# Kernel tuning notes

Hardware: AMD Instinct MI355X
Metric: run time of the kernel (lower is better)

Reference implementation:

```python
import jax, jax.numpy as jnp
import numpy as np

N_EMBD = 512
N_HEAD = 8
N_INPUTS = 3
HEAD = N_EMBD // N_HEAD


def setup_inputs() -> dict:
    key = jax.random.key(0)
    ks = jax.random.split(key, 12)
    B, T1, T2, C, NI = 2, 2048, 2048, N_EMBD, N_INPUTS
    s = 0.02
    return {
        "x": jax.random.normal(ks[0], (B, T1, C), jnp.float32),
        "y": jax.random.normal(ks[1], (NI, B, T2, C), jnp.float32),
        "Wq": jax.random.normal(ks[2], (C, C), jnp.float32) * s,
        "bq": jnp.zeros((C,), jnp.float32),
        "Wk": jax.random.normal(ks[3], (NI, C, C), jnp.float32) * s,
        "bk": jnp.zeros((NI, C), jnp.float32),
        "Wv": jax.random.normal(ks[4], (NI, C, C), jnp.float32) * s,
        "bv": jnp.zeros((NI, C), jnp.float32),
        "Wp": jax.random.normal(ks[5], (C, C), jnp.float32) * s,
        "bp": jnp.zeros((C,), jnp.float32),
    }


def reference(x, y, Wq, bq, Wk, bk, Wv, bv, Wp, bp):
    B, T1, C = x.shape
    H, D = N_HEAD, HEAD
    # q: [B,H,T1,D], pre-scaled by 1/sqrt(D) as in the original
    q = (x @ Wq + bq).reshape(B, T1, H, D).transpose(0, 2, 1, 3)
    q = q / jnp.sqrt(jnp.asarray(D, q.dtype))
    out = jnp.zeros_like(q)
    for i in range(N_INPUTS):  # small fixed loop over distinct K/V sources
        yi = y[i]
        T2 = yi.shape[1]
        k = (yi @ Wk[i] + bk[i]).reshape(B, T2, H, D).transpose(0, 2, 1, 3)
        v = (yi @ Wv[i] + bv[i]).reshape(B, T2, H, D).transpose(0, 2, 1, 3)
        attn = jax.nn.softmax(jnp.einsum('bhqd,bhkd->bhqk', q, k), axis=-1)
        out = out + jnp.einsum('bhqk,bhkd->bhqd', attn, v)
    out = out.transpose(0, 2, 1, 3).reshape(B, T1, C)
    return out @ Wp + bp
```

## Files before the change

### kernel.cpp

```cpp
#include <hip/hip_runtime.h>

typedef __attribute__((ext_vector_type(8))) __bf16 bf16x8;
typedef __attribute__((ext_vector_type(4))) __bf16 bf16x4;
typedef __attribute__((ext_vector_type(4))) float f32x4;
typedef __attribute__((ext_vector_type(8))) unsigned short us8;

__device__ __forceinline__ unsigned short f2b(float f) {
    unsigned int u = __builtin_bit_cast(unsigned int, f);
    u = (u + 0x7fffu + ((u >> 16) & 1u)) >> 16;
    return (unsigned short)u;
}
__device__ __forceinline__ float b2f(unsigned short u) {
    return __builtin_bit_cast(float, (unsigned int)u << 16);
}
__device__ __forceinline__ float exp2fast(float x) {
    return __builtin_amdgcn_exp2f(x);
}
__device__ __forceinline__ void gload16(const void* g, void* l) {
    __builtin_amdgcn_global_load_lds(
        (const __attribute__((address_space(1))) unsigned int*)g,
        (__attribute__((address_space(3))) unsigned int*)l, 16, 0, 0);
}

#define LOG2E 1.44269504088896f

__global__ void prep_w(const float* __restrict__ Wq, const float* __restrict__ Wk,
                       const float* __restrict__ Wv, const float* __restrict__ Wp,
                       unsigned short* __restrict__ Wt) {
    __shared__ float tile[64][65];
    int w = blockIdx.z;
    const float* src = (w == 0) ? Wq
                     : (w < 4)  ? Wk + (size_t)(w - 1) * 512 * 512
                     : (w < 7)  ? Wv + (size_t)(w - 4) * 512 * 512
                                : Wp;
    int n0 = blockIdx.x * 64, k0 = blockIdx.y * 64;
    int t = threadIdx.x;
    int rr = t >> 4, c4 = (t & 15) * 4;
#pragma unroll
    for (int j = 0; j < 4; j++) {
        int r = rr + j * 16;
        float4 v = *(const float4*)(src + (size_t)(k0 + r) * 512 + n0 + c4);
        tile[r][c4 + 0] = v.x; tile[r][c4 + 1] = v.y;
        tile[r][c4 + 2] = v.z; tile[r][c4 + 3] = v.w;
    }
    __syncthreads();
#pragma unroll
    for (int j = 0; j < 4; j++) {
        int rn = rr + j * 16;
        ushort4 o;
        o.x = f2b(tile[c4 + 0][rn]); o.y = f2b(tile[c4 + 1][rn]);
        o.z = f2b(tile[c4 + 2][rn]); o.w = f2b(tile[c4 + 3][rn]);
        *(ushort4*)(Wt + (size_t)w * 512 * 512 + (size_t)(n0 + rn) * 512 + k0 + c4) = o;
    }
}

template <int MODE>
__global__ __launch_bounds__(256, 3) void gemm_k(
    const float* __restrict__ x, const float* __restrict__ y,
    const unsigned short* __restrict__ Wt,
    const float* __restrict__ bq, const float* __restrict__ bk, const float* __restrict__ bv,
    unsigned short* __restrict__ Qb, unsigned short* __restrict__ Kb, unsigned short* __restrict__ Vb,
    const unsigned short* __restrict__ aob, const float* __restrict__ bp, float* __restrict__ outf) {
    __shared__ unsigned short As[128 * 64];
    __shared__ unsigned short Bs[128 * 64];

    int bid = blockIdx.x;
    int CHUNK = (MODE == 0) ? 112 : 16;
    int w = (bid & 7) * CHUNK + (bid >> 3);
    int z, mq, nq;
    if (MODE == 0) {
        z = w >> 7;
        int rem = w & 127;
        mq = rem >> 2; nq = rem & 3;
    } else {
        z = 0; mq = w >> 2; nq = w & 3;
    }

    const float* A = nullptr;
    const unsigned short* W;
    const float* bias;
    unsigned short* outb = nullptr;
    float scale = 1.f;
    if (MODE == 0) {
        if (z == 0) {
            A = x; W = Wt; bias = bq; outb = Qb; scale = 0.125f * LOG2E;
        } else if (z < 4) {
            int i = z - 1;
            A = y + (size_t)i * 4096 * 512;
            W = Wt + (size_t)z * 512 * 512;
            bias = bk + i * 512;
            outb = Kb + (size_t)i * 4096 * 512;
        } else {
            int i = z - 4;
            A = y + (size_t)i * 4096 * 512;
            W = Wt + (size_t)z * 512 * 512;
            bias = bv + i * 512;
            outb = Vb + (size_t)i * 4096 * 512;
        }
    } else {
        W = Wt + (size_t)7 * 512 * 512; bias = bp;
    }

    int m0 = mq * 128, n0 = nq * 128;
    int t = threadIdx.x;
    int lane = t & 63, wid = t >> 6;
    int lg = lane >> 4, lr = lane & 15;
    int wm = wid >> 1, wn = wid & 1;
    int ssl = lane & 7, srow8 = lane >> 3;

    f32x4 acc[4][4];
    const f32x4 zf = {0.f, 0.f, 0.f, 0.f};
#pragma unroll
    for (int mi = 0; mi < 4; mi++)
#pragma unroll
        for (int ni = 0; ni < 4; ni++) acc[mi][ni] = zf;

    for (int kt = 0; kt < 8; ++kt) {
        float4 av[8];
        if (MODE == 0) {
#pragma unroll
            for (int j = 0; j < 8; j++) {
                int c = t + 256 * j;
                int row = c >> 4, kq = c & 15;
                av[j] = *(const float4*)(A + (size_t)(m0 + row) * 512 + kt * 64 + kq * 4);
            }
        }
        __syncthreads();
#pragma unroll
        for (int j = 0; j < 4; j++) {
            int row = (j * 4 + wid) * 8 + srow8;
            gload16(W + (size_t)(n0 + row) * 512 + kt * 64 + ((ssl ^ (row & 7)) * 8),
                    Bs + (j * 4 + wid) * 512);
        }
        if (MODE == 0) {
#pragma unroll
            for (int j = 0; j < 8; j++) {
                int c = t + 256 * j;
                int row = c >> 4, kq = c & 15;
                float4 v = av[j];
                bf16x4 o4 = {(__bf16)v.x, (__bf16)v.y, (__bf16)v.z, (__bf16)v.w};
                *(bf16x4*)(As + row * 64 + (((kq >> 1) ^ (row & 7)) * 8) + (kq & 1) * 4) = o4;
            }
        } else {
#pragma unroll
            for (int j = 0; j < 4; j++) {
                int c = t + 256 * j;
                int row = c >> 3, sl = c & 7;
                const unsigned short* p0 = aob + (size_t)(m0 + row) * 512 + kt * 64 + sl * 8;
                us8 a0 = *(const us8*)p0;
                us8 a1 = *(const us8*)(p0 + (size_t)4096 * 512);
                us8 a2 = *(const us8*)(p0 + (size_t)2 * 4096 * 512);
                bf16x8 o8;
#pragma unroll
                for (int e = 0; e < 8; e++)
                    o8[e] = (__bf16)(b2f(a0[e]) + b2f(a1[e]) + b2f(a2[e]));
                *(bf16x8*)(As + row * 64 + ((sl ^ (row & 7)) * 8)) = o8;
            }
        }
        __syncthreads();

        bf16x8 af[4][2];
#pragma unroll
        for (int mi = 0; mi < 4; mi++)
#pragma unroll
            for (int kk = 0; kk < 2; kk++) {
                int row = wm * 64 + mi * 16 + lr;
                int sl = (kk * 4 + lg) ^ (row & 7);
                af[mi][kk] = *(const bf16x8*)(As + row * 64 + sl * 8);
            }
        __builtin_amdgcn_s_setprio(1);
#pragma unroll
        for (int ni = 0; ni < 4; ni++)
#pragma unroll
            for (int kk = 0; kk < 2; kk++) {
                int row = wn * 64 + ni * 16 + lr;
                int sl = (kk * 4 + lg) ^ (row & 7);
                bf16x8 bf = *(const bf16x8*)(Bs + row * 64 + sl * 8);
#pragma unroll
                for (int mi = 0; mi < 4; mi++)
                    acc[mi][ni] = __builtin_amdgcn_mfma_f32_16x16x32_bf16(af[mi][kk], bf, acc[mi][ni], 0, 0, 0);
            }
        __builtin_amdgcn_s_setprio(0);
    }

#pragma unroll
    for (int ni = 0; ni < 4; ni++) {
        int col = n0 + wn * 64 + ni * 16 + lr;
        float bb = bias[col];
#pragma unroll
        for (int mi = 0; mi < 4; mi++) {
            int row0 = m0 + wm * 64 + mi * 16 + lg * 4;
#pragma unroll
            for (int r = 0; r < 4; r++) {
                float v = (acc[mi][ni][r] + bb) * scale;
                if (MODE == 0)
                    outb[(size_t)(row0 + r) * 512 + col] = __builtin_bit_cast(unsigned short, (__bf16)v);
                else
                    outf[(size_t)(row0 + r) * 512 + col] = v;
            }
        }
    }
}

__global__ void transpose_v(const unsigned short* __restrict__ Vb,
                            unsigned short* __restrict__ Vt) {
    __shared__ unsigned short tile[64][68];
    int i = blockIdx.z, bh = blockIdx.y, t20 = blockIdx.x * 64;
    int b = bh >> 3, h = bh & 7;
    int t = threadIdx.x;
    int rr = t >> 4, c4 = (t & 15) * 4;
    const unsigned short* src = Vb + (size_t)i * 4096 * 512 + (size_t)(b * 2048 + t20) * 512 + h * 64;
#pragma unroll
    for (int j = 0; j < 4; j++) {
        int r = rr + j * 16;
        ushort4 v = *(const ushort4*)(src + (size_t)r * 512 + c4);
        tile[r][c4 + 0] = v.x; tile[r][c4 + 1] = v.y;
        tile[r][c4 + 2] = v.z; tile[r][c4 + 3] = v.w;
    }
    __syncthreads();
    unsigned short* dst = Vt + ((size_t)(i * 16 + bh) * 64) * 2048 + t20;
#pragma unroll
    for (int j = 0; j < 4; j++) {
        int d = rr + j * 16;
        ushort4 o;
        o.x = tile[c4 + 0][d]; o.y = tile[c4 + 1][d];
        o.z = tile[c4 + 2][d]; o.w = tile[c4 + 3][d];
        *(ushort4*)(dst + (size_t)d * 2048 + c4) = o;
    }
}

__global__ __launch_bounds__(256, 4) void attn_k(
    const unsigned short* __restrict__ Qb, const unsigned short* __restrict__ Kb,
    const unsigned short* __restrict__ Vt, unsigned short* __restrict__ attoutB) {
    __shared__ unsigned short Ks[2][64 * 64];
    __shared__ unsigned short Vs[2][64 * 64];
    __shared__ unsigned short Ps[4][16 * 64];

    int bid = blockIdx.x;
    int w = (bid & 7) * 192 + (bid >> 3);
    int q0 = (w & 31) * 64;
    int bh = (w >> 5) & 15;
    int i = w >> 9;
    int b = bh >> 3, h = bh & 7;
    int t = threadIdx.x, lane = t & 63, wid = t >> 6;
    int lg = lane >> 4, lr = lane & 15;
    int x7 = lr & 7;
    int ssl = lane & 7, srow = wid * 16 + (lane >> 3);
    int sswz = (ssl ^ (srow & 7)) * 8;

    const unsigned short* kb = Kb + ((size_t)i * 4096 + b * 2048) * 512 + h * 64;
    const unsigned short* vt = Vt + ((size_t)(i * 16 + bh) * 64) * 2048;

    const unsigned short* qp = Qb + (size_t)(b * 2048 + q0 + wid * 16 + lr) * 512 + h * 64 + lg * 8;
    bf16x8 qf0 = *(const bf16x8*)(qp);
    bf16x8 qf1 = *(const bf16x8*)(qp + 32);

    int fb0 = lr * 128 + ((lg ^ x7) << 4);
    int fb1 = fb0 ^ 64;
    int pwb = (lr * 128 + lg * 8) ^ (x7 << 4);
    int prd0 = (lr * 128 + lg * 16) ^ (x7 << 4);
    int prd1 = prd0 ^ 64;

    const f32x4 zf = {0.f, 0.f, 0.f, 0.f};
    f32x4 o[4];
#pragma unroll
    for (int ni = 0; ni < 4; ni++) o[ni] = zf;
    float l = 0.f;
    char* Pw = (char*)Ps[wid];

#define STAGE(buf, t20)                                                          \
    do {                                                                         \
        gload16(kb + (size_t)((t20) + srow) * 512 + sswz, Ks[buf] + (wid * 2 + 0) * 512);      \
        gload16(kb + (size_t)((t20) + srow + 8) * 512 + sswz, Ks[buf] + (wid * 2 + 1) * 512);  \
        gload16(vt + (size_t)srow * 2048 + (t20) + sswz, Vs[buf] + (wid * 2 + 0) * 512);       \
        gload16(vt + (size_t)(srow + 8) * 2048 + (t20) + sswz, Vs[buf] + (wid * 2 + 1) * 512); \
    } while (0)

    STAGE(0, 0);
    for (int tt = 0; tt < 32; tt++) {
        int cur = tt & 1;
        __syncthreads();
        if (tt + 1 < 32) STAGE(cur ^ 1, (tt + 1) * 64);

        const char* Ksc = (const char*)Ks[cur];
        const char* Vsc = (const char*)Vs[cur];

        f32x4 s[4];
#pragma unroll
        for (int ni = 0; ni < 4; ni++) s[ni] = zf;
        __builtin_amdgcn_s_setprio(1);
#pragma unroll
        for (int kk = 0; kk < 2; kk++) {
            bf16x8 q = kk ? qf1 : qf0;
            int fb = kk ? fb1 : fb0;
#pragma unroll
            for (int ni = 0; ni < 4; ni++) {
                bf16x8 kf = *(const bf16x8*)(Ksc + fb + ni * 2048);
                s[ni] = __builtin_amdgcn_mfma_f32_16x16x32_bf16(kf, q, s[ni], 0, 0, 0);
            }
        }
        __builtin_amdgcn_s_setprio(0);

#pragma unroll
        for (int ni = 0; ni < 4; ni++) {
            float e0 = exp2fast(s[ni][0]);
            float e1 = exp2fast(s[ni][1]);
            float e2 = exp2fast(s[ni][2]);
            float e3 = exp2fast(s[ni][3]);
            l += (e0 + e1) + (e2 + e3);
            bf16x4 pk = {(__bf16)e0, (__bf16)e1, (__bf16)e2, (__bf16)e3};
            *(bf16x4*)(Pw + (pwb ^ (ni * 32))) = pk;
        }

        asm volatile("s_waitcnt lgkmcnt(0)" ::: "memory");
        __builtin_amdgcn_sched_barrier(0);

        bf16x8 pa0 = *(const bf16x8*)(Pw + prd0);
        bf16x8 pa1 = *(const bf16x8*)(Pw + prd1);
        __builtin_amdgcn_s_setprio(1);
#pragma unroll
        for (int ni = 0; ni < 4; ni++) {
            bf16x8 v0 = *(const bf16x8*)(Vsc + fb0 + ni * 2048);
            bf16x8 v1 = *(const bf16x8*)(Vsc + fb1 + ni * 2048);
            o[ni] = __builtin_amdgcn_mfma_f32_16x16x32_bf16(v0, pa0, o[ni], 0, 0, 0);
            o[ni] = __builtin_amdgcn_mfma_f32_16x16x32_bf16(v1, pa1, o[ni], 0, 0, 0);
        }
        __builtin_amdgcn_s_setprio(0);
    }
#undef STAGE

    l += __shfl_xor(l, 16);
    l += __shfl_xor(l, 32);
    float rl = 1.f / l;
    unsigned short* ao = attoutB + (size_t)i * 4096 * 512
                       + (size_t)(b * 2048 + q0 + wid * 16 + lr) * 512 + h * 64 + lg * 4;
#pragma unroll
    for (int ni = 0; ni < 4; ni++) {
        bf16x4 ov = {(__bf16)(o[ni][0] * rl), (__bf16)(o[ni][1] * rl),
                     (__bf16)(o[ni][2] * rl), (__bf16)(o[ni][3] * rl)};
        *(bf16x4*)(ao + ni * 16) = ov;
    }
}

extern "C" void kernel_launch(void* const* d_in, const int* in_sizes, int n_in,
                              void* d_out, int out_size, void* d_ws, size_t ws_size,
                              hipStream_t stream) {
    (void)in_sizes; (void)n_in; (void)out_size; (void)ws_size;
    const float* x  = (const float*)d_in[0];
    const float* y  = (const float*)d_in[1];
    const float* Wq = (const float*)d_in[2];
    const float* bq = (const float*)d_in[3];
    const float* Wk = (const float*)d_in[4];
    const float* bk = (const float*)d_in[5];
    const float* Wv = (const float*)d_in[6];
    const float* bv = (const float*)d_in[7];
    const float* Wp = (const float*)d_in[8];
    const float* bp = (const float*)d_in[9];
    float* out = (float*)d_out;

    char* ws = (char*)d_ws;
    const size_t MB = 1024 * 1024;
    unsigned short* Wt = (unsigned short*)(ws);
    unsigned short* Qb = (unsigned short*)(ws + 4 * MB);
    unsigned short* Kb = (unsigned short*)(ws + 8 * MB);
    unsigned short* Vb = (unsigned short*)(ws + 20 * MB);
    unsigned short* Vt = (unsigned short*)(ws + 32 * MB);
    unsigned short* attoutB = (unsigned short*)(ws + 20 * MB);

    prep_w<<<dim3(8, 8, 8), 256, 0, stream>>>(Wq, Wk, Wv, Wp, Wt);
    gemm_k<0><<<896, 256, 0, stream>>>(x, y, Wt, bq, bk, bv, Qb, Kb, Vb,
                                       nullptr, nullptr, nullptr);
    transpose_v<<<dim3(32, 16, 3), 256, 0, stream>>>(Vb, Vt);
    attn_k<<<1536, 256, 0, stream>>>(Qb, Kb, Vt, attoutB);
    gemm_k<1><<<128, 256, 0, stream>>>(nullptr, nullptr, Wt, nullptr, nullptr, nullptr,
                                       nullptr, nullptr, nullptr, attoutB, bp, out);
}
```

Baseline: 230.6 us.

## Pre-convert activations to bf16 and use 512-thread attention blocks

A new prep kernel converts x and y to bf16 once, so the QKV GEMM can stage A tiles with direct global-to-LDS loads instead of loading fp32 into registers and converting. The GEMM's MFMA loop is reordered per k-slice to reduce live A fragments, and its occupancy hint is raised. The attention kernel now uses 512-thread blocks covering 128 queries, so each K/V tile is shared by 8 waves instead of 4. This adds an extra kernel launch and a full bf16 copy of the activations in exchange for lighter GEMM staging and more K/V reuse.

```diff
diff --git a/kernel.cpp b/kernel.cpp
--- a/kernel.cpp
+++ b/kernel.cpp
@@ -23,6 +23,18 @@
 }
 
 #define LOG2E 1.44269504088896f
+
+__global__ void prep_a(const float* __restrict__ x, const float* __restrict__ y,
+                       unsigned short* __restrict__ Ab) {
+    size_t e = ((size_t)blockIdx.x * 256 + threadIdx.x) * 8;
+    const size_t XN = (size_t)2 * 2048 * 512;
+    const float* src = (e < XN) ? x + e : y + (e - XN);
+    float4 a = *(const float4*)src;
+    float4 b = *(const float4*)(src + 4);
+    bf16x8 o = {(__bf16)a.x, (__bf16)a.y, (__bf16)a.z, (__bf16)a.w,
+                (__bf16)b.x, (__bf16)b.y, (__bf16)b.z, (__bf16)b.w};
+    *(bf16x8*)(Ab + e) = o;
+}
 
 __global__ void prep_w(const float* __restrict__ Wq, const float* __restrict__ Wk,
                        const float* __restrict__ Wv, const float* __restrict__ Wp,
@@ -55,8 +67,8 @@
 }
 
 template <int MODE>
-__global__ __launch_bounds__(256, 3) void gemm_k(
-    const float* __restrict__ x, const float* __restrict__ y,
+__global__ __launch_bounds__(256, MODE == 0 ? 4 : 3) void gemm_k(
+    const unsigned short* __restrict__ Ab,
     const unsigned short* __restrict__ Wt,
     const float* __restrict__ bq, const float* __restrict__ bk, const float* __restrict__ bv,
     unsigned short* __restrict__ Qb, unsigned short* __restrict__ Kb, unsigned short* __restrict__ Vb,
@@ -76,26 +88,21 @@
         z = 0; mq = w >> 2; nq = w & 3;
     }
 
-    const float* A = nullptr;
+    const unsigned short* A = nullptr;
     const unsigned short* W;
     const float* bias;
     unsigned short* outb = nullptr;
     float scale = 1.f;
     if (MODE == 0) {
+        int slice = (z < 4) ? z : z - 3;
+        A = Ab + (size_t)slice * 4096 * 512;
+        W = Wt + (size_t)z * 512 * 512;
         if (z == 0) {
-            A = x; W = Wt; bias = bq; outb = Qb; scale = 0.125f * LOG2E;
+            bias = bq; outb = Qb; scale = 0.125f * LOG2E;
         } else if (z < 4) {
-            int i = z - 1;
-            A = y + (size_t)i * 4096 * 512;
-            W = Wt + (size_t)z * 512 * 512;
-            bias = bk + i * 512;
-            outb = Kb + (size_t)i * 4096 * 512;
+            bias = bk + (z - 1) * 512; outb = Kb + (size_t)(z - 1) * 4096 * 512;
         } else {
-            int i = z - 4;
-            A = y + (size_t)i * 4096 * 512;
-            W = Wt + (size_t)z * 512 * 512;
-            bias = bv + i * 512;
-            outb = Vb + (size_t)i * 4096 * 512;
+            bias = bv + (z - 4) * 512; outb = Vb + (size_t)(z - 4) * 4096 * 512;
         }
     } else {
         W = Wt + (size_t)7 * 512 * 512; bias = bp;
@@ -116,15 +123,6 @@
         for (int ni = 0; ni < 4; ni++) acc[mi][ni] = zf;
 
     for (int kt = 0; kt < 8; ++kt) {
-        float4 av[8];
-        if (MODE == 0) {
-#pragma unroll
-            for (int j = 0; j < 8; j++) {
-                int c = t + 256 * j;
-                int row = c >> 4, kq = c & 15;
-                av[j] = *(const float4*)(A + (size_t)(m0 + row) * 512 + kt * 64 + kq * 4);
-            }
-        }
         __syncthreads();
 #pragma unroll
         for (int j = 0; j < 4; j++) {
@@ -134,12 +132,10 @@
         }
         if (MODE == 0) {
 #pragma unroll
-            for (int j = 0; j < 8; j++) {
-                int c = t + 256 * j;
-                int row = c >> 4, kq = c & 15;
-                float4 v = av[j];
-                bf16x4 o4 = {(__bf16)v.x, (__bf16)v.y, (__bf16)v.z, (__bf16)v.w};
-                *(bf16x4*)(As + row * 64 + (((kq >> 1) ^ (row & 7)) * 8) + (kq & 1) * 4) = o4;
+            for (int j = 0; j < 4; j++) {
+                int row = (j * 4 + wid) * 8 + srow8;
+                gload16(A + (size_t)(m0 + row) * 512 + kt * 64 + ((ssl ^ (row & 7)) * 8),
+                        As + (j * 4 + wid) * 512);
             }
         } else {
 #pragma unroll
@@ -159,27 +155,26 @@
         }
         __syncthreads();
 
-        bf16x8 af[4][2];
-#pragma unroll
-        for (int mi = 0; mi < 4; mi++)
-#pragma unroll
-            for (int kk = 0; kk < 2; kk++) {
+        __builtin_amdgcn_s_setprio(1);
+#pragma unroll
+        for (int kk = 0; kk < 2; kk++) {
+            bf16x8 af[4];
+#pragma unroll
+            for (int mi = 0; mi < 4; mi++) {
                 int row = wm * 64 + mi * 16 + lr;
                 int sl = (kk * 4 + lg) ^ (row & 7);
-                af[mi][kk] = *(const bf16x8*)(As + row * 64 + sl * 8);
-            }
-        __builtin_amdgcn_s_setprio(1);
-#pragma unroll
-        for (int ni = 0; ni < 4; ni++)
-#pragma unroll
-            for (int kk = 0; kk < 2; kk++) {
+                af[mi] = *(const bf16x8*)(As + row * 64 + sl * 8);
+            }
+#pragma unroll
+            for (int ni = 0; ni < 4; ni++) {
                 int row = wn * 64 + ni * 16 + lr;
                 int sl = (kk * 4 + lg) ^ (row & 7);
                 bf16x8 bf = *(const bf16x8*)(Bs + row * 64 + sl * 8);
 #pragma unroll
                 for (int mi = 0; mi < 4; mi++)
-                    acc[mi][ni] = __builtin_amdgcn_mfma_f32_16x16x32_bf16(af[mi][kk], bf, acc[mi][ni], 0, 0, 0);
-            }
+                    acc[mi][ni] = __builtin_amdgcn_mfma_f32_16x16x32_bf16(af[mi], bf, acc[mi][ni], 0, 0, 0);
+            }
+        }
         __builtin_amdgcn_s_setprio(0);
     }
 
@@ -229,23 +224,24 @@
     }
 }
 
-__global__ __launch_bounds__(256, 4) void attn_k(
+__global__ __launch_bounds__(512, 6) void attn_k(
     const unsigned short* __restrict__ Qb, const unsigned short* __restrict__ Kb,
     const unsigned short* __restrict__ Vt, unsigned short* __restrict__ attoutB) {
     __shared__ unsigned short Ks[2][64 * 64];
     __shared__ unsigned short Vs[2][64 * 64];
-    __shared__ unsigned short Ps[4][16 * 64];
+    __shared__ unsigned short Ps[8][16 * 64];
 
     int bid = blockIdx.x;
-    int w = (bid & 7) * 192 + (bid >> 3);
-    int q0 = (w & 31) * 64;
-    int bh = (w >> 5) & 15;
-    int i = w >> 9;
+    int w = (bid & 7) * 96 + (bid >> 3);
+    int qt = w & 15;
+    int bh = (w >> 4) & 15;
+    int i = w >> 8;
     int b = bh >> 3, h = bh & 7;
+    int q0 = qt * 128;
     int t = threadIdx.x, lane = t & 63, wid = t >> 6;
     int lg = lane >> 4, lr = lane & 15;
     int x7 = lr & 7;
-    int ssl = lane & 7, srow = wid * 16 + (lane >> 3);
+    int ssl = lane & 7, srow = wid * 8 + (lane >> 3);
     int sswz = (ssl ^ (srow & 7)) * 8;
 
     const unsigned short* kb = Kb + ((size_t)i * 4096 + b * 2048) * 512 + h * 64;
@@ -268,12 +264,10 @@
     float l = 0.f;
     char* Pw = (char*)Ps[wid];
 
-#define STAGE(buf, t20)                                                          \
-    do {                                                                         \
-        gload16(kb + (size_t)((t20) + srow) * 512 + sswz, Ks[buf] + (wid * 2 + 0) * 512);      \
-        gload16(kb + (size_t)((t20) + srow + 8) * 512 + sswz, Ks[buf] + (wid * 2 + 1) * 512);  \
-        gload16(vt + (size_t)srow * 2048 + (t20) + sswz, Vs[buf] + (wid * 2 + 0) * 512);       \
-        gload16(vt + (size_t)(srow + 8) * 2048 + (t20) + sswz, Vs[buf] + (wid * 2 + 1) * 512); \
+#define STAGE(buf, t20)                                                      \
+    do {                                                                     \
+        gload16(kb + (size_t)((t20) + srow) * 512 + sswz, Ks[buf] + wid * 512); \
+        gload16(vt + (size_t)srow * 2048 + (t20) + sswz, Vs[buf] + wid * 512);  \
     } while (0)
 
     STAGE(0, 0);
@@ -366,12 +360,14 @@
     unsigned short* Vb = (unsigned short*)(ws + 20 * MB);
     unsigned short* Vt = (unsigned short*)(ws + 32 * MB);
     unsigned short* attoutB = (unsigned short*)(ws + 20 * MB);
-
+    unsigned short* Ab = (unsigned short*)(ws + 44 * MB);
+
+    prep_a<<<4096, 256, 0, stream>>>(x, y, Ab);
     prep_w<<<dim3(8, 8, 8), 256, 0, stream>>>(Wq, Wk, Wv, Wp, Wt);
-    gemm_k<0><<<896, 256, 0, stream>>>(x, y, Wt, bq, bk, bv, Qb, Kb, Vb,
+    gemm_k<0><<<896, 256, 0, stream>>>(Ab, Wt, bq, bk, bv, Qb, Kb, Vb,
                                        nullptr, nullptr, nullptr);
     transpose_v<<<dim3(32, 16, 3), 256, 0, stream>>>(Vb, Vt);
-    attn_k<<<1536, 256, 0, stream>>>(Qb, Kb, Vt, attoutB);
-    gemm_k<1><<<128, 256, 0, stream>>>(nullptr, nullptr, Wt, nullptr, nullptr, nullptr,
+    attn_k<<<768, 512, 0, stream>>>(Qb, Kb, Vt, attoutB);
+    gemm_k<1><<<128, 256, 0, stream>>>(nullptr, Wt, nullptr, nullptr, nullptr,
                                        nullptr, nullptr, nullptr, attoutB, bp, out);
 }
```

Measured after the change: 219.4 us. -4.9%, faster.
